# Kernel optimization log

Measured on AMD Instinct MI355X. Metric: run time of the kernel, lower is better.

## Reference

```python
import jax, jax.numpy as jnp
import numpy as np

THRESHOLD = 0.5
NEG_POS = 3
ALPHA = 1.0


def cxcy_to_xy(b):
    return jnp.concatenate([b[:, :2] - b[:, 2:] / 2, b[:, :2] + b[:, 2:] / 2], axis=-1)


def xy_to_cxcy(b):
    return jnp.concatenate([(b[:, :2] + b[:, 2:]) / 2, b[:, 2:] - b[:, :2]], axis=-1)


def encode_bboxes(cxcy, priors_cxcy):
    # standard SSD encoding with variances (0.1, 0.2)
    g_cxcy = (cxcy[:, :2] - priors_cxcy[:, :2]) / (priors_cxcy[:, 2:] / 10.0)
    g_wh = jnp.log(cxcy[:, 2:] / priors_cxcy[:, 2:]) * 5.0
    return jnp.concatenate([g_cxcy, g_wh], axis=-1)


def compute_iou(a, b):
    # a: [n,4] xyxy, b: [m,4] xyxy -> [n,m]
    lt = jnp.maximum(a[:, None, :2], b[None, :, :2])
    rb = jnp.minimum(a[:, None, 2:], b[None, :, 2:])
    wh = jnp.clip(rb - lt, 0.0)
    inter = wh[..., 0] * wh[..., 1]
    area_a = (a[:, 2] - a[:, 0]) * (a[:, 3] - a[:, 1])
    area_b = (b[:, 2] - b[:, 0]) * (b[:, 3] - b[:, 1])
    return inter / (area_a[:, None] + area_b[None, :] - inter)


def setup_inputs() -> dict:
    key = jax.random.key(0)
    k1, k2, k3, k4, k5, k6 = jax.random.split(key, 6)
    B, D, C, O = 128, 8732, 21, 16
    loc_pred = jax.random.normal(k1, (B, D, 4), dtype=jnp.float32)
    cls_pred = jax.random.normal(k2, (B, D, C), dtype=jnp.float32)
    # valid gt boxes: xmin<xmax, ymin<ymax
    p = jax.random.uniform(k3, (B, O, 4), dtype=jnp.float32)
    x1 = jnp.minimum(p[..., 0], p[..., 2])
    x2 = jnp.maximum(p[..., 0], p[..., 2]) + 1e-2
    y1 = jnp.minimum(p[..., 1], p[..., 3])
    y2 = jnp.maximum(p[..., 1], p[..., 3]) + 1e-2
    gt_boxes = jnp.stack([x1, y1, x2, y2], axis=-1)
    gt_labels = jax.random.randint(k4, (B, O), 1, C)
    # priors in cxcywh, w/h in (0.05, 0.5)
    cxy = jax.random.uniform(k5, (D, 2), dtype=jnp.float32)
    wh = jax.random.uniform(k6, (D, 2), dtype=jnp.float32) * 0.45 + 0.05
    default_boxes = jnp.concatenate([cxy, wh], axis=-1)
    return {"loc_pred": loc_pred, "cls_pred": cls_pred, "gt_boxes": gt_boxes,
            "gt_labels": gt_labels, "default_boxes": default_boxes}


def _match_and_losses(loc_pred, cls_pred, gt_boxes, gt_labels, default_boxes):
    B, D, C = cls_pred.shape
    O = gt_boxes.shape[1]
    db_xy = cxcy_to_xy(default_boxes)

    def match_one(boxes_i, labels_i):
        iou = compute_iou(boxes_i, db_xy)                 # [O, D]
        best_truth_overlap = iou.max(axis=0)              # [D]
        best_truth_idx = iou.argmax(axis=0)               # [D]
        best_default_idx = iou.argmax(axis=1)             # [O]
        best_truth_idx = best_truth_idx.at[best_default_idx].set(jnp.arange(O))
        best_truth_overlap = best_truth_overlap.at[best_default_idx].set(1.0)
        labels = labels_i[best_truth_idx]                 # [D]
        labels = jnp.where(best_truth_overlap < THRESHOLD, 0, labels)
        matched_xy = boxes_i[best_truth_idx]              # [D,4]
        loc = encode_bboxes(xy_to_cxcy(matched_xy), default_boxes)
        return loc, labels

    loc_t, conf_t = jax.vmap(match_one)(gt_boxes, gt_labels)  # [B,D,4], [B,D]
    loc_t = jax.lax.stop_gradient(loc_t)  # targets carry no grad (requires_grad=False)

    pos = conf_t > 0                                      # [B,D]
    n_positive = pos.sum(axis=1)                          # [B]
    n_pos_total = n_positive.sum()

    # SmoothL1 (beta=1), mean over positive elements (num_pos * 4)
    diff = loc_pred - loc_t
    ad = jnp.abs(diff)
    sl1 = jnp.where(ad < 1.0, 0.5 * diff * diff, ad - 0.5)
    loc_loss = (sl1 * pos[..., None]).sum() / (n_pos_total.astype(jnp.float32) * 4.0)

    # per-element cross entropy
    logp = jax.nn.log_softmax(cls_pred, axis=-1)          # [B,D,C]
    ce = -jnp.take_along_axis(logp, conf_t[..., None], axis=-1)[..., 0]  # [B,D]

    conf_pos_sum = (ce * pos).sum()
    neg_loss = jnp.where(pos, 0.0, ce)
    neg_sorted = -jnp.sort(-neg_loss, axis=1)             # descending per row
    ranks = jnp.arange(D)[None, :]
    hard = ranks < (NEG_POS * n_positive)[:, None]
    conf_neg_sum = (neg_sorted * hard).sum()
    conf_loss = (conf_neg_sum + conf_pos_sum) / n_pos_total.astype(jnp.float32)

    return ALPHA * loc_loss + conf_loss


def reference(loc_pred, cls_pred, gt_boxes, gt_labels, default_boxes):
    return _match_and_losses(loc_pred, cls_pred, gt_boxes, gt_labels, default_boxes)
```

## Files before the change

### kernel.cpp

```cpp
#include <hip/hip_runtime.h>

#define BB 128
#define DD 8732
#define OO 16
#define CC 21
#define CH 16
#define CHUNK 546
#define NG4 2183
#define NBLK_C 9
#define NLB (BB * NBLK_C)
#define NV 35

__device__ __forceinline__ float smoothl1(float d) {
    float ad = fabsf(d);
    return (ad < 1.0f) ? 0.5f * d * d : ad - 0.5f;
}

__global__ __launch_bounds__(256) void match_a(
    const float4* __restrict__ gt_boxes,
    const float4* __restrict__ db,
    unsigned long long* __restrict__ partial,
    unsigned* __restrict__ bpk,
    int* __restrict__ done_counter)
{
    const int b = blockIdx.y, ch = blockIdx.x, tid = threadIdx.x;
    if (b == 0 && ch == 0 && tid == 0) *done_counter = 0;

    __shared__ float s_ax1[OO], s_ay1[OO], s_ax2[OO], s_ay2[OO], s_area[OO];
    __shared__ unsigned long long s_keys[OO][257];

    if (tid < OO) {
        float4 g = gt_boxes[b * OO + tid];
        s_ax1[tid] = g.x; s_ay1[tid] = g.y; s_ax2[tid] = g.z; s_ay2[tid] = g.w;
        s_area[tid] = (g.z - g.x) * (g.w - g.y);
    }
    __syncthreads();

    unsigned long long key[OO];
    #pragma unroll
    for (int o = 0; o < OO; ++o) key[o] = 0ull;

    const int d0 = ch * CHUNK;
    const int dend = min(d0 + CHUNK, DD);
    for (int d = d0 + tid; d < dend; d += 256) {
        float4 p = db[d];
        float px1 = p.x - p.z * 0.5f, py1 = p.y - p.w * 0.5f;
        float px2 = p.x + p.z * 0.5f, py2 = p.y + p.w * 0.5f;
        float area_b = (px2 - px1) * (py2 - py1);
        unsigned dl = (unsigned)(DD - 1 - d);
        float best = -1.0f; int bi = 0;
        #pragma unroll
        for (int o = 0; o < OO; ++o) {
            float w = fmaxf(fminf(s_ax2[o], px2) - fmaxf(s_ax1[o], px1), 0.0f);
            float h = fmaxf(fminf(s_ay2[o], py2) - fmaxf(s_ay1[o], py1), 0.0f);
            float inter = w * h;
            float uni = s_area[o] + area_b - inter;
            float iou = inter * __builtin_amdgcn_rcpf(uni);
            unsigned long long kk = ((unsigned long long)__float_as_uint(iou) << 32) | dl;
            if (kk > key[o]) key[o] = kk;
            if (iou > best) { best = iou; bi = o; }
        }
        bpk[(size_t)b * DD + d] = (__float_as_uint(best) & 0xFFFFFF00u) | (unsigned)bi;
    }
    #pragma unroll
    for (int o = 0; o < OO; ++o) s_keys[o][tid] = key[o];
    __syncthreads();

    const int o = tid >> 4, j = tid & 15;
    unsigned long long mx = s_keys[o][j];
    #pragma unroll
    for (int m = 1; m < 16; ++m) {
        unsigned long long v = s_keys[o][j + 16 * m];
        if (v > mx) mx = v;
    }
    #pragma unroll
    for (int off = 8; off; off >>= 1) {
        unsigned long long v = __shfl_xor(mx, off, 16);
        if (v > mx) mx = v;
    }
    if (j == 0) partial[((size_t)b * OO + o) * CH + ch] = mx;
}

__global__ __launch_bounds__(256) void fused_main(
    const float4* __restrict__ loc_pred,
    const float*  __restrict__ cls,
    const float4* __restrict__ gt_boxes,
    const int*    __restrict__ gt_labels,
    const float4* __restrict__ db,
    const unsigned long long* __restrict__ partial,
    const unsigned* __restrict__ bpk,
    float* __restrict__ ce_neg,
    float* __restrict__ part_sl1,
    int*   __restrict__ part_np,
    float* __restrict__ part_ce)
{
    const int b = blockIdx.y, jb = blockIdx.x, tid = threadIdx.x;
    const int g = jb * 256 + tid;
    __shared__ float s_ax1[OO], s_ay1[OO], s_ax2[OO], s_ay2[OO];
    __shared__ int   s_lab[OO], s_bdi[OO];
    __shared__ unsigned char s_ovr[1024];
    __shared__ float s_f[8];
    __shared__ int   s_i[4];

    if (tid < OO) {
        float4 gg = gt_boxes[b * OO + tid];
        s_ax1[tid] = gg.x; s_ay1[tid] = gg.y; s_ax2[tid] = gg.z; s_ay2[tid] = gg.w;
        s_lab[tid] = gt_labels[b * OO + tid];
    }
    {
        unsigned long long k = partial[(size_t)b * (OO * CH) + tid];
        #pragma unroll
        for (int off = 8; off; off >>= 1) {
            unsigned long long v = __shfl_xor(k, off, 16);
            if (v > k) k = v;
        }
        if ((tid & 15) == 0) s_bdi[tid >> 4] = DD - 1 - (int)(k & 0xffffffffu);
    }
    ((unsigned*)s_ovr)[tid] = 0xFFFFFFFFu;
    __syncthreads();
    if (tid == 0) {
        #pragma unroll
        for (int o = 0; o < OO; ++o) {
            int ds = s_bdi[o] - jb * 1024;
            if (0 <= ds && ds < 1024) s_ovr[ds] = (unsigned char)o;
        }
    }
    __syncthreads();

    float sl1 = 0.0f, cepos = 0.0f; int npos = 0;
    if (g < NG4) {
        const int row0 = g * 4;
        const size_t gi4 = (size_t)b * DD + row0;
        float e[84];
        const float4* src = (const float4*)(cls + gi4 * CC);
        #pragma unroll
        for (int jv = 0; jv < 21; ++jv) {
            float4 q = src[jv];
            e[4*jv+0] = q.x; e[4*jv+1] = q.y; e[4*jv+2] = q.z; e[4*jv+3] = q.w;
        }
        uint4 pk4 = *(const uint4*)(bpk + gi4);
        unsigned pks[4] = {pk4.x, pk4.y, pk4.z, pk4.w};
        float out[4];
        #pragma unroll
        for (int r = 0; r < 4; ++r) {
            const int row = row0 + r;
            unsigned upk = pks[r];
            int bi = (int)(upk & 0xFFu);
            float best = __uint_as_float(upk & 0xFFFFFF00u);
            int ov = s_ovr[4 * tid + r];
            if (ov != 0xFF) { bi = ov; best = 1.0f; }
            int lab = (best < 0.5f) ? 0 : s_lab[bi];

            float m = e[21*r];
            #pragma unroll
            for (int c = 1; c < CC; ++c) m = fmaxf(m, e[21*r + c]);
            float s = 0.0f;
            #pragma unroll
            for (int c = 0; c < CC; ++c) s += __expf(e[21*r + c] - m);
            float xl = (lab == 0) ? e[21*r] : cls[(gi4 + r) * CC + lab];
            float ce = m + __logf(s) - xl;

            if (lab > 0) {
                npos += 1; cepos += ce;
                float ax1 = s_ax1[bi], ay1 = s_ay1[bi], ax2 = s_ax2[bi], ay2 = s_ay2[bi];
                float cx = (ax1 + ax2) * 0.5f, cy = (ay1 + ay2) * 0.5f;
                float w = ax2 - ax1, h = ay2 - ay1;
                float4 p = db[row];
                float gx = (cx - p.x) / (p.z / 10.0f);
                float gy = (cy - p.y) / (p.w / 10.0f);
                float gw = __logf(w / p.z) * 5.0f;
                float gh = __logf(h / p.w) * 5.0f;
                float4 lp = loc_pred[gi4 + r];
                sl1 += smoothl1(lp.x - gx) + smoothl1(lp.y - gy)
                     + smoothl1(lp.z - gw) + smoothl1(lp.w - gh);
                out[r] = 0.0f;
            } else {
                out[r] = ce;
            }
        }
        *(float4*)(ce_neg + gi4) = make_float4(out[0], out[1], out[2], out[3]);
    }

    #pragma unroll
    for (int off = 32; off; off >>= 1) {
        sl1   += __shfl_xor(sl1, off);
        cepos += __shfl_xor(cepos, off);
        npos  += __shfl_xor(npos, off);
    }
    const int w = tid >> 6;
    if ((tid & 63) == 0) { s_f[w*2+0] = sl1; s_f[w*2+1] = cepos; s_i[w] = npos; }
    __syncthreads();
    if (tid == 0) {
        float sv = 0, cp = 0; int np = 0;
        #pragma unroll
        for (int q = 0; q < 4; ++q) { sv += s_f[q*2+0]; cp += s_f[q*2+1]; np += s_i[q]; }
        const int pi = b * NBLK_C + jb;
        part_sl1[pi] = sv;
        part_ce[pi]  = cp;
        part_np[pi]  = np;
    }
}

__global__ __launch_bounds__(256) void topk_final(
    const float* __restrict__ ce_neg,
    const int*   __restrict__ part_np,
    const float* __restrict__ part_sl1,
    const float* __restrict__ part_ce,
    float* __restrict__ conf_neg_part,
    int*   __restrict__ done_counter,
    float* __restrict__ out)
{
    const int b = blockIdx.x, tid = threadIdx.x;
    __shared__ int      hist[256];
    __shared__ unsigned s_pk[2];
    __shared__ float    s_f[12];
    __shared__ int      s_c[4];
    __shared__ int      s_last;

    int np = 0;
    #pragma unroll
    for (int jb = 0; jb < NBLK_C; ++jb) np += part_np[b * NBLK_C + jb];
    int k0 = 3 * np;
    if (k0 > DD) k0 = DD;

    float row = 0.0f;
    if (k0 > 0) {
        unsigned kx[NV];
        #pragma unroll
        for (int q = 0; q < NV; ++q) {
            int d = q * 256 + tid;
            float v = (d < DD) ? ce_neg[(size_t)b * DD + d] : 0.0f;
            unsigned u = __float_as_uint(v);
            kx[q] = u ^ ((unsigned)((int)u >> 31) | 0x80000000u);
        }

        unsigned prefix = 0u; int k = k0;
        #pragma unroll
        for (int p = 0; p < 4; ++p) {
            const int shift = 24 - 8 * p;
            hist[tid] = 0;
            __syncthreads();
            #pragma unroll
            for (int q = 0; q < NV; ++q) {
                if (p == 0 || ((kx[q] ^ prefix) >> (shift + 8)) == 0u)
                    atomicAdd(&hist[(kx[q] >> shift) & 255], 1);
            }
            __syncthreads();
            if (tid < 64) {
                int h0 = hist[255 - 4*tid], h1 = hist[254 - 4*tid],
                    h2 = hist[253 - 4*tid], h3 = hist[252 - 4*tid];
                int sl = h0 + h1 + h2 + h3;
                int run = sl;
                #pragma unroll
                for (int off = 1; off < 64; off <<= 1) {
                    int v = __shfl_up(run, off);
                    if (tid >= off) run += v;
                }
                int pre = run - sl;
                if (pre < k && k <= pre + sl) {
                    int hh[4] = {h0, h1, h2, h3};
                    int c = pre, byte = -1, knew = 0;
                    #pragma unroll
                    for (int j = 0; j < 4; ++j) {
                        if (byte < 0 && c + hh[j] >= k) { byte = 255 - 4*tid - j; knew = k - c; }
                        c += hh[j];
                    }
                    s_pk[0] = prefix | ((unsigned)byte << shift);
                    s_pk[1] = (unsigned)knew;
                }
            }
            __syncthreads();
            prefix = s_pk[0]; k = (int)s_pk[1];
        }

        unsigned vb = (prefix & 0x80000000u) ? (prefix ^ 0x80000000u) : ~prefix;
        float vk = __uint_as_float(vb);

        float ssum = 0.0f; int cgt = 0;
        #pragma unroll
        for (int q = 0; q < NV; ++q) {
            if (kx[q] > prefix) {
                unsigned u = (kx[q] & 0x80000000u) ? (kx[q] ^ 0x80000000u) : ~kx[q];
                ssum += __uint_as_float(u);
                ++cgt;
            }
        }
        #pragma unroll
        for (int off = 32; off; off >>= 1) { ssum += __shfl_xor(ssum, off); cgt += __shfl_xor(cgt, off); }
        if ((tid & 63) == 0) { s_f[tid >> 6] = ssum; s_c[tid >> 6] = cgt; }
        __syncthreads();
        row = s_f[0]+s_f[1]+s_f[2]+s_f[3]
            + (float)(k0 - (s_c[0]+s_c[1]+s_c[2]+s_c[3])) * vk;
    }

    if (tid == 0) {
        conf_neg_part[b] = row;
        __threadfence();
        int prev = atomicAdd(done_counter, 1);
        s_last = (prev == BB - 1) ? 1 : 0;
    }
    __syncthreads();
    if (s_last) {
        __threadfence();
        float loc = 0.0f, cp = 0.0f; int npt = 0;
        for (int i = tid; i < NLB; i += 256) {
            loc += part_sl1[i]; cp += part_ce[i]; npt += part_np[i];
        }
        float cn = (tid < BB) ? conf_neg_part[tid] : 0.0f;
        #pragma unroll
        for (int off = 32; off; off >>= 1) {
            loc += __shfl_xor(loc, off);
            cp  += __shfl_xor(cp, off);
            cn  += __shfl_xor(cn, off);
            npt += __shfl_xor(npt, off);
        }
        const int w = tid >> 6;
        if ((tid & 63) == 0) { s_f[w*3+0] = loc; s_f[w*3+1] = cp; s_f[w*3+2] = cn; s_c[w] = npt; }
        __syncthreads();
        if (tid == 0) {
            float L = 0, P = 0, N = 0; int T = 0;
            #pragma unroll
            for (int q = 0; q < 4; ++q) { L += s_f[q*3]; P += s_f[q*3+1]; N += s_f[q*3+2]; T += s_c[q]; }
            float npf = (float)T;
            out[0] = L / (npf * 4.0f) + (N + P) / npf;
        }
    }
}

extern "C" void kernel_launch(void* const* d_in, const int* in_sizes, int n_in,
                              void* d_out, int out_size, void* d_ws, size_t ws_size,
                              hipStream_t stream) {
    (void)in_sizes; (void)n_in; (void)out_size; (void)ws_size;
    const float4* loc_pred  = (const float4*)d_in[0];
    const float*  cls_pred  = (const float*)d_in[1];
    const float4* gt_boxes  = (const float4*)d_in[2];
    const int*    gt_labels = (const int*)d_in[3];
    const float4* db        = (const float4*)d_in[4];

    char* ws = (char*)d_ws;
    size_t off = 0;
    auto alloc = [&](size_t bytes) { char* p = ws + off; off = (off + bytes + 15) & ~(size_t)15; return p; };

    unsigned long long* partial = (unsigned long long*)alloc((size_t)BB * OO * CH * 8);
    float* ce_neg        = (float*)alloc((size_t)BB * DD * 4);
    unsigned* bpk        = (unsigned*)alloc((size_t)BB * DD * 4);
    float* part_sl1      = (float*)alloc((size_t)NLB * 4);
    int*   part_np       = (int*)alloc((size_t)NLB * 4);
    float* part_ce       = (float*)alloc((size_t)NLB * 4);
    float* conf_neg_part = (float*)alloc((size_t)BB * 4);
    int*   done_counter  = (int*)alloc(sizeof(int));

    match_a<<<dim3(CH, BB), 256, 0, stream>>>(gt_boxes, db, partial, bpk,
                                              done_counter);
    fused_main<<<dim3(NBLK_C, BB), 256, 0, stream>>>(loc_pred, cls_pred, gt_boxes,
                                                     gt_labels, db, partial, bpk,
                                                     ce_neg, part_sl1, part_np, part_ce);
    topk_final<<<BB, 256, 0, stream>>>(ce_neg, part_np, part_sl1, part_ce,
                                       conf_neg_part, done_counter, (float*)d_out);
}
```

Before: 67.43 us.

## Fuse IoU matching into main loss kernel and patch forced matches in top-k kernel

Removes the separate matching kernel and its per-prior best-match buffer. The main kernel now computes IoU and best-gt per row in registers and reduces each gt's best prior via a global 64-bit atomicMax. Because forced per-gt matches are only known once all blocks finish, the top-k kernel recomputes those up to 16 rows per image and applies delta corrections to the loss sums, count and ce_neg before selection. This saves a launch and a global round trip, at the cost of a memset, atomics, and extra serial work in the top-k kernel.

```diff
diff --git a/kernel.cpp b/kernel.cpp
--- a/kernel.cpp
+++ b/kernel.cpp
@@ -4,8 +4,6 @@
 #define DD 8732
 #define OO 16
 #define CC 21
-#define CH 16
-#define CHUNK 546
 #define NG4 2183
 #define NBLK_C 9
 #define NLB (BB * NBLK_C)
@@ -16,79 +14,13 @@
     return (ad < 1.0f) ? 0.5f * d * d : ad - 0.5f;
 }
 
-__global__ __launch_bounds__(256) void match_a(
-    const float4* __restrict__ gt_boxes,
-    const float4* __restrict__ db,
-    unsigned long long* __restrict__ partial,
-    unsigned* __restrict__ bpk,
-    int* __restrict__ done_counter)
-{
-    const int b = blockIdx.y, ch = blockIdx.x, tid = threadIdx.x;
-    if (b == 0 && ch == 0 && tid == 0) *done_counter = 0;
-
-    __shared__ float s_ax1[OO], s_ay1[OO], s_ax2[OO], s_ay2[OO], s_area[OO];
-    __shared__ unsigned long long s_keys[OO][257];
-
-    if (tid < OO) {
-        float4 g = gt_boxes[b * OO + tid];
-        s_ax1[tid] = g.x; s_ay1[tid] = g.y; s_ax2[tid] = g.z; s_ay2[tid] = g.w;
-        s_area[tid] = (g.z - g.x) * (g.w - g.y);
-    }
-    __syncthreads();
-
-    unsigned long long key[OO];
-    #pragma unroll
-    for (int o = 0; o < OO; ++o) key[o] = 0ull;
-
-    const int d0 = ch * CHUNK;
-    const int dend = min(d0 + CHUNK, DD);
-    for (int d = d0 + tid; d < dend; d += 256) {
-        float4 p = db[d];
-        float px1 = p.x - p.z * 0.5f, py1 = p.y - p.w * 0.5f;
-        float px2 = p.x + p.z * 0.5f, py2 = p.y + p.w * 0.5f;
-        float area_b = (px2 - px1) * (py2 - py1);
-        unsigned dl = (unsigned)(DD - 1 - d);
-        float best = -1.0f; int bi = 0;
-        #pragma unroll
-        for (int o = 0; o < OO; ++o) {
-            float w = fmaxf(fminf(s_ax2[o], px2) - fmaxf(s_ax1[o], px1), 0.0f);
-            float h = fmaxf(fminf(s_ay2[o], py2) - fmaxf(s_ay1[o], py1), 0.0f);
-            float inter = w * h;
-            float uni = s_area[o] + area_b - inter;
-            float iou = inter * __builtin_amdgcn_rcpf(uni);
-            unsigned long long kk = ((unsigned long long)__float_as_uint(iou) << 32) | dl;
-            if (kk > key[o]) key[o] = kk;
-            if (iou > best) { best = iou; bi = o; }
-        }
-        bpk[(size_t)b * DD + d] = (__float_as_uint(best) & 0xFFFFFF00u) | (unsigned)bi;
-    }
-    #pragma unroll
-    for (int o = 0; o < OO; ++o) s_keys[o][tid] = key[o];
-    __syncthreads();
-
-    const int o = tid >> 4, j = tid & 15;
-    unsigned long long mx = s_keys[o][j];
-    #pragma unroll
-    for (int m = 1; m < 16; ++m) {
-        unsigned long long v = s_keys[o][j + 16 * m];
-        if (v > mx) mx = v;
-    }
-    #pragma unroll
-    for (int off = 8; off; off >>= 1) {
-        unsigned long long v = __shfl_xor(mx, off, 16);
-        if (v > mx) mx = v;
-    }
-    if (j == 0) partial[((size_t)b * OO + o) * CH + ch] = mx;
-}
-
-__global__ __launch_bounds__(256) void fused_main(
+__global__ __launch_bounds__(256) void fused_all(
     const float4* __restrict__ loc_pred,
     const float*  __restrict__ cls,
     const float4* __restrict__ gt_boxes,
     const int*    __restrict__ gt_labels,
     const float4* __restrict__ db,
-    const unsigned long long* __restrict__ partial,
-    const unsigned* __restrict__ bpk,
+    unsigned long long* __restrict__ partial,
     float* __restrict__ ce_neg,
     float* __restrict__ part_sl1,
     int*   __restrict__ part_np,
@@ -96,40 +28,93 @@
 {
     const int b = blockIdx.y, jb = blockIdx.x, tid = threadIdx.x;
     const int g = jb * 256 + tid;
-    __shared__ float s_ax1[OO], s_ay1[OO], s_ax2[OO], s_ay2[OO];
-    __shared__ int   s_lab[OO], s_bdi[OO];
-    __shared__ unsigned char s_ovr[1024];
+    __shared__ float s_ax1[OO], s_ay1[OO], s_ax2[OO], s_ay2[OO], s_area[OO];
+    __shared__ int   s_lab[OO];
+    __shared__ unsigned long long s_keys[8][257];
     __shared__ float s_f[8];
     __shared__ int   s_i[4];
 
     if (tid < OO) {
         float4 gg = gt_boxes[b * OO + tid];
         s_ax1[tid] = gg.x; s_ay1[tid] = gg.y; s_ax2[tid] = gg.z; s_ay2[tid] = gg.w;
+        s_area[tid] = (gg.z - gg.x) * (gg.w - gg.y);
         s_lab[tid] = gt_labels[b * OO + tid];
     }
-    {
-        unsigned long long k = partial[(size_t)b * (OO * CH) + tid];
+    __syncthreads();
+
+    unsigned long long key[OO];
+    #pragma unroll
+    for (int o = 0; o < OO; ++o) key[o] = 0ull;
+    int lab_r[4] = {0, 0, 0, 0};
+    int bi_r[4]  = {0, 0, 0, 0};
+
+    const int row0 = g * 4;
+    if (g < NG4) {
+        #pragma unroll
+        for (int r = 0; r < 4; ++r) {
+            const int d = row0 + r;
+            float4 p = db[d];
+            float px1 = p.x - p.z * 0.5f, py1 = p.y - p.w * 0.5f;
+            float px2 = p.x + p.z * 0.5f, py2 = p.y + p.w * 0.5f;
+            float area_b = (px2 - px1) * (py2 - py1);
+            unsigned dl = (unsigned)(DD - 1 - d);
+            float best = -1.0f; int bi = 0;
+            #pragma unroll
+            for (int o = 0; o < OO; ++o) {
+                float w = fmaxf(fminf(s_ax2[o], px2) - fmaxf(s_ax1[o], px1), 0.0f);
+                float h = fmaxf(fminf(s_ay2[o], py2) - fmaxf(s_ay1[o], py1), 0.0f);
+                float inter = w * h;
+                float uni = s_area[o] + area_b - inter;
+                float iou = inter * __builtin_amdgcn_rcpf(uni);
+                unsigned long long kk = ((unsigned long long)__float_as_uint(iou) << 32) | dl;
+                if (kk > key[o]) key[o] = kk;
+                if (iou > best) { best = iou; bi = o; }
+            }
+            lab_r[r] = (best < 0.5f) ? 0 : s_lab[bi];
+            bi_r[r]  = bi;
+        }
+    }
+
+    #pragma unroll
+    for (int o = 0; o < 8; ++o) s_keys[o][tid] = key[o];
+    __syncthreads();
+    if (tid < 128) {
+        const int o = tid >> 4, j = tid & 15;
+        unsigned long long mx = s_keys[o][j];
+        #pragma unroll
+        for (int m = 1; m < 16; ++m) {
+            unsigned long long v = s_keys[o][j + 16 * m];
+            if (v > mx) mx = v;
+        }
         #pragma unroll
         for (int off = 8; off; off >>= 1) {
-            unsigned long long v = __shfl_xor(k, off, 16);
-            if (v > k) k = v;
-        }
-        if ((tid & 15) == 0) s_bdi[tid >> 4] = DD - 1 - (int)(k & 0xffffffffu);
-    }
-    ((unsigned*)s_ovr)[tid] = 0xFFFFFFFFu;
-    __syncthreads();
-    if (tid == 0) {
-        #pragma unroll
-        for (int o = 0; o < OO; ++o) {
-            int ds = s_bdi[o] - jb * 1024;
-            if (0 <= ds && ds < 1024) s_ovr[ds] = (unsigned char)o;
-        }
-    }
-    __syncthreads();
+            unsigned long long v = __shfl_xor(mx, off, 16);
+            if (v > mx) mx = v;
+        }
+        if (j == 0) atomicMax(&partial[b * OO + o], mx);
+    }
+    __syncthreads();
+    #pragma unroll
+    for (int o = 0; o < 8; ++o) s_keys[o][tid] = key[8 + o];
+    __syncthreads();
+    if (tid < 128) {
+        const int o = tid >> 4, j = tid & 15;
+        unsigned long long mx = s_keys[o][j];
+        #pragma unroll
+        for (int m = 1; m < 16; ++m) {
+            unsigned long long v = s_keys[o][j + 16 * m];
+            if (v > mx) mx = v;
+        }
+        #pragma unroll
+        for (int off = 8; off; off >>= 1) {
+            unsigned long long v = __shfl_xor(mx, off, 16);
+            if (v > mx) mx = v;
+        }
+        if (j == 0) atomicMax(&partial[b * OO + 8 + o], mx);
+    }
 
     float sl1 = 0.0f, cepos = 0.0f; int npos = 0;
     if (g < NG4) {
-        const int row0 = g * 4;
         const size_t gi4 = (size_t)b * DD + row0;
         float e[84];
         const float4* src = (const float4*)(cls + gi4 * CC);
@@ -138,19 +123,10 @@
             float4 q = src[jv];
             e[4*jv+0] = q.x; e[4*jv+1] = q.y; e[4*jv+2] = q.z; e[4*jv+3] = q.w;
         }
-        uint4 pk4 = *(const uint4*)(bpk + gi4);
-        unsigned pks[4] = {pk4.x, pk4.y, pk4.z, pk4.w};
         float out[4];
         #pragma unroll
         for (int r = 0; r < 4; ++r) {
-            const int row = row0 + r;
-            unsigned upk = pks[r];
-            int bi = (int)(upk & 0xFFu);
-            float best = __uint_as_float(upk & 0xFFFFFF00u);
-            int ov = s_ovr[4 * tid + r];
-            if (ov != 0xFF) { bi = ov; best = 1.0f; }
-            int lab = (best < 0.5f) ? 0 : s_lab[bi];
-
+            const int lab = lab_r[r];
             float m = e[21*r];
             #pragma unroll
             for (int c = 1; c < CC; ++c) m = fmaxf(m, e[21*r + c]);
@@ -159,13 +135,13 @@
             for (int c = 0; c < CC; ++c) s += __expf(e[21*r + c] - m);
             float xl = (lab == 0) ? e[21*r] : cls[(gi4 + r) * CC + lab];
             float ce = m + __logf(s) - xl;
-
             if (lab > 0) {
                 npos += 1; cepos += ce;
+                const int bi = bi_r[r];
                 float ax1 = s_ax1[bi], ay1 = s_ay1[bi], ax2 = s_ax2[bi], ay2 = s_ay2[bi];
                 float cx = (ax1 + ax2) * 0.5f, cy = (ay1 + ay2) * 0.5f;
                 float w = ax2 - ax1, h = ay2 - ay1;
-                float4 p = db[row];
+                float4 p = db[row0 + r];
                 float gx = (cx - p.x) / (p.z / 10.0f);
                 float gy = (cy - p.y) / (p.w / 10.0f);
                 float gw = __logf(w / p.z) * 5.0f;
@@ -202,10 +178,19 @@
 }
 
 __global__ __launch_bounds__(256) void topk_final(
-    const float* __restrict__ ce_neg,
+    const float*  __restrict__ cls,
+    const float4* __restrict__ loc_pred,
+    const float4* __restrict__ gt_boxes,
+    const int*    __restrict__ gt_labels,
+    const float4* __restrict__ db,
+    const unsigned long long* __restrict__ partial,
+    float* __restrict__ ce_neg,
+    const float* __restrict__ part_sl1,
     const int*   __restrict__ part_np,
-    const float* __restrict__ part_sl1,
     const float* __restrict__ part_ce,
+    float* __restrict__ img_sl1,
+    float* __restrict__ img_ce,
+    int*   __restrict__ img_np,
     float* __restrict__ conf_neg_part,
     int*   __restrict__ done_counter,
     float* __restrict__ out)
@@ -215,12 +200,109 @@
     __shared__ unsigned s_pk[2];
     __shared__ float    s_f[12];
     __shared__ int      s_c[4];
+    __shared__ int      s_bdi[OO], s_lab[OO];
+    __shared__ float    s_ax1[OO], s_ay1[OO], s_ax2[OO], s_ay2[OO], s_area[OO];
+    __shared__ float    s_dsl1, s_dce;
+    __shared__ int      s_dnp, s_np;
+    __shared__ float    s_isl1, s_ice;
     __shared__ int      s_last;
 
-    int np = 0;
-    #pragma unroll
-    for (int jb = 0; jb < NBLK_C; ++jb) np += part_np[b * NBLK_C + jb];
-    int k0 = 3 * np;
+    if (tid < OO) {
+        float4 gg = gt_boxes[b * OO + tid];
+        s_ax1[tid] = gg.x; s_ay1[tid] = gg.y; s_ax2[tid] = gg.z; s_ay2[tid] = gg.w;
+        s_area[tid] = (gg.z - gg.x) * (gg.w - gg.y);
+        s_lab[tid] = gt_labels[b * OO + tid];
+        s_bdi[tid] = DD - 1 - (int)(partial[b * OO + tid] & 0xffffffffu);
+    }
+    __syncthreads();
+
+    float dsl1 = 0.0f, dce = 0.0f; int dnp = 0;
+    if (tid < OO) {
+        const int R = s_bdi[tid];
+        bool winner = true;
+        for (int o2 = tid + 1; o2 < OO; ++o2)
+            if (s_bdi[o2] == R) winner = false;
+        if (winner) {
+            float4 p = db[R];
+            float px1 = p.x - p.z * 0.5f, py1 = p.y - p.w * 0.5f;
+            float px2 = p.x + p.z * 0.5f, py2 = p.y + p.w * 0.5f;
+            float area_b = (px2 - px1) * (py2 - py1);
+            float best = -1.0f; int bi = 0;
+            #pragma unroll
+            for (int o = 0; o < OO; ++o) {
+                float w = fmaxf(fminf(s_ax2[o], px2) - fmaxf(s_ax1[o], px1), 0.0f);
+                float h = fmaxf(fminf(s_ay2[o], py2) - fmaxf(s_ay1[o], py1), 0.0f);
+                float inter = w * h;
+                float uni = s_area[o] + area_b - inter;
+                float iou = inter * __builtin_amdgcn_rcpf(uni);
+                if (iou > best) { best = iou; bi = o; }
+            }
+            int lab0 = (best < 0.5f) ? 0 : s_lab[bi];
+
+            const float* x = cls + ((size_t)b * DD + R) * CC;
+            float m = x[0];
+            #pragma unroll
+            for (int c = 1; c < CC; ++c) m = fmaxf(m, x[c]);
+            float s = 0.0f;
+            #pragma unroll
+            for (int c = 0; c < CC; ++c) s += __expf(x[c] - m);
+            float lse = m + __logf(s);
+            float4 lp = loc_pred[(size_t)b * DD + R];
+
+            if (lab0 > 0) {
+                dce -= (lse - x[lab0]);
+                dnp -= 1;
+                float ax1 = s_ax1[bi], ay1 = s_ay1[bi], ax2 = s_ax2[bi], ay2 = s_ay2[bi];
+                float cx = (ax1 + ax2) * 0.5f, cy = (ay1 + ay2) * 0.5f;
+                float w = ax2 - ax1, h = ay2 - ay1;
+                float gx = (cx - p.x) / (p.z / 10.0f);
+                float gy = (cy - p.y) / (p.w / 10.0f);
+                float gw = __logf(w / p.z) * 5.0f;
+                float gh = __logf(h / p.w) * 5.0f;
+                dsl1 -= smoothl1(lp.x - gx) + smoothl1(lp.y - gy)
+                      + smoothl1(lp.z - gw) + smoothl1(lp.w - gh);
+            } else {
+                ce_neg[(size_t)b * DD + R] = 0.0f;
+            }
+            dce += (lse - x[s_lab[tid]]);
+            dnp += 1;
+            {
+                float ax1 = s_ax1[tid], ay1 = s_ay1[tid], ax2 = s_ax2[tid], ay2 = s_ay2[tid];
+                float cx = (ax1 + ax2) * 0.5f, cy = (ay1 + ay2) * 0.5f;
+                float w = ax2 - ax1, h = ay2 - ay1;
+                float gx = (cx - p.x) / (p.z / 10.0f);
+                float gy = (cy - p.y) / (p.w / 10.0f);
+                float gw = __logf(w / p.z) * 5.0f;
+                float gh = __logf(h / p.w) * 5.0f;
+                dsl1 += smoothl1(lp.x - gx) + smoothl1(lp.y - gy)
+                      + smoothl1(lp.z - gw) + smoothl1(lp.w - gh);
+            }
+        }
+    }
+    if (tid < 64) {
+        #pragma unroll
+        for (int off = 8; off; off >>= 1) {
+            dsl1 += __shfl_xor(dsl1, off, 16);
+            dce  += __shfl_xor(dce, off, 16);
+            dnp  += __shfl_xor(dnp, off, 16);
+        }
+        if (tid == 0) { s_dsl1 = dsl1; s_dce = dce; s_dnp = dnp; }
+    }
+    __syncthreads();
+
+    if (tid == 0) {
+        float a = 0, c2 = 0; int n = 0;
+        #pragma unroll
+        for (int j = 0; j < NBLK_C; ++j) {
+            a  += part_sl1[b * NBLK_C + j];
+            c2 += part_ce[b * NBLK_C + j];
+            n  += part_np[b * NBLK_C + j];
+        }
+        s_isl1 = a + s_dsl1; s_ice = c2 + s_dce; s_np = n + s_dnp;
+    }
+    __syncthreads();
+
+    int k0 = 3 * s_np;
     if (k0 > DD) k0 = DD;
 
     float row = 0.0f;
@@ -233,7 +315,6 @@
             unsigned u = __float_as_uint(v);
             kx[q] = u ^ ((unsigned)((int)u >> 31) | 0x80000000u);
         }
-
         unsigned prefix = 0u; int k = k0;
         #pragma unroll
         for (int p = 0; p < 4; ++p) {
@@ -272,7 +353,6 @@
             __syncthreads();
             prefix = s_pk[0]; k = (int)s_pk[1];
         }
-
         unsigned vb = (prefix & 0x80000000u) ? (prefix ^ 0x80000000u) : ~prefix;
         float vk = __uint_as_float(vb);
 
@@ -295,6 +375,7 @@
 
     if (tid == 0) {
         conf_neg_part[b] = row;
+        img_sl1[b] = s_isl1; img_ce[b] = s_ice; img_np[b] = s_np;
         __threadfence();
         int prev = atomicAdd(done_counter, 1);
         s_last = (prev == BB - 1) ? 1 : 0;
@@ -302,11 +383,11 @@
     __syncthreads();
     if (s_last) {
         __threadfence();
-        float loc = 0.0f, cp = 0.0f; int npt = 0;
-        for (int i = tid; i < NLB; i += 256) {
-            loc += part_sl1[i]; cp += part_ce[i]; npt += part_np[i];
-        }
-        float cn = (tid < BB) ? conf_neg_part[tid] : 0.0f;
+        float loc = 0.0f, cp = 0.0f, cn = 0.0f; int npt = 0;
+        if (tid < BB) {
+            loc = img_sl1[tid]; cp = img_ce[tid];
+            cn = conf_neg_part[tid]; npt = img_np[tid];
+        }
         #pragma unroll
         for (int off = 32; off; off >>= 1) {
             loc += __shfl_xor(loc, off);
@@ -341,20 +422,24 @@
     size_t off = 0;
     auto alloc = [&](size_t bytes) { char* p = ws + off; off = (off + bytes + 15) & ~(size_t)15; return p; };
 
-    unsigned long long* partial = (unsigned long long*)alloc((size_t)BB * OO * CH * 8);
+    unsigned long long* partial = (unsigned long long*)alloc((size_t)BB * OO * 8);
+    int*   done_counter  = (int*)alloc(16);
     float* ce_neg        = (float*)alloc((size_t)BB * DD * 4);
-    unsigned* bpk        = (unsigned*)alloc((size_t)BB * DD * 4);
     float* part_sl1      = (float*)alloc((size_t)NLB * 4);
     int*   part_np       = (int*)alloc((size_t)NLB * 4);
     float* part_ce       = (float*)alloc((size_t)NLB * 4);
+    float* img_sl1       = (float*)alloc((size_t)BB * 4);
+    float* img_ce        = (float*)alloc((size_t)BB * 4);
+    int*   img_np        = (int*)alloc((size_t)BB * 4);
     float* conf_neg_part = (float*)alloc((size_t)BB * 4);
-    int*   done_counter  = (int*)alloc(sizeof(int));
-
-    match_a<<<dim3(CH, BB), 256, 0, stream>>>(gt_boxes, db, partial, bpk,
-                                              done_counter);
-    fused_main<<<dim3(NBLK_C, BB), 256, 0, stream>>>(loc_pred, cls_pred, gt_boxes,
-                                                     gt_labels, db, partial, bpk,
-                                                     ce_neg, part_sl1, part_np, part_ce);
-    topk_final<<<BB, 256, 0, stream>>>(ce_neg, part_np, part_sl1, part_ce,
-                                       conf_neg_part, done_counter, (float*)d_out);
+
+    hipMemsetAsync(partial, 0, (size_t)BB * OO * 8 + 16, stream);
+
+    fused_all<<<dim3(NBLK_C, BB), 256, 0, stream>>>(loc_pred, cls_pred, gt_boxes,
+                                                    gt_labels, db, partial,
+                                                    ce_neg, part_sl1, part_np, part_ce);
+    topk_final<<<BB, 256, 0, stream>>>(cls_pred, loc_pred, gt_boxes, gt_labels, db,
+                                       partial, ce_neg, part_sl1, part_np, part_ce,
+                                       img_sl1, img_ce, img_np, conf_neg_part,
+                                       done_counter, (float*)d_out);
 }
```

Measured after the change: 67.39 us. Within noise of the previous version (-0.1%).
